# Optimization experiments

Measured on AMD Instinct MI355X. Metric: run time of the kernel, lower is better.

Reference implementation:

```python
import jax, jax.numpy as jnp
import numpy as np

EMBED = 1024
HEADS = 16
HEAD_DIM = EMBED // HEADS


def setup_inputs() -> dict:
    key = jax.random.key(0)
    k_x, k_qkv, k_ow, k_ob = jax.random.split(key, 4)
    B, N, D = 4, 2048, EMBED
    x = jax.random.normal(k_x, (B, N, D), dtype=jnp.float32)
    # nn.Linear stores weight as [out, in]; apply as x @ W.T
    s_in = 1.0 / np.sqrt(D)
    W_qkv = jax.random.uniform(k_qkv, (3 * D, D), dtype=jnp.float32, minval=-s_in, maxval=s_in)
    W_out = jax.random.uniform(k_ow, (D, D), dtype=jnp.float32, minval=-s_in, maxval=s_in)
    b_out = jax.random.uniform(k_ob, (D,), dtype=jnp.float32, minval=-s_in, maxval=s_in)
    return {"x": x, "W_qkv": W_qkv, "W_out": W_out, "b_out": b_out}


def reference(x, W_qkv, W_out, b_out):
    B, N, D = x.shape
    H, HD = HEADS, HEAD_DIM
    qkv = jnp.einsum("bnd,ed->bne", x, W_qkv)          # [B, N, 3D]
    qkv = qkv.reshape(B, N, 3, H, HD).transpose(2, 0, 3, 1, 4)  # [3, B, H, N, HD]
    q, k, v = qkv[0], qkv[1], qkv[2]
    scale = HD ** -0.5
    scores = jnp.einsum("bhnd,bhmd->bhnm", q, k) * scale  # [B, H, N, N]
    attn = jax.nn.softmax(scores, axis=-1)
    out = jnp.einsum("bhnm,bhmd->bhnd", attn, v)          # [B, H, N, HD]
    out = out.transpose(0, 2, 1, 3).reshape(B, N, D)
    return jnp.einsum("bnd,ed->bne", out, W_out) + b_out
```

## Files before the change

### kernel.cpp

```cpp
#include <hip/hip_runtime.h>
#include <hip/hip_bf16.h>
#include <stdint.h>

typedef float f32x4 __attribute__((ext_vector_type(4)));
typedef __bf16 v8bf __attribute__((ext_vector_type(8)));
typedef __bf16 v4bf __attribute__((ext_vector_type(4)));
typedef unsigned short u16x8 __attribute__((ext_vector_type(8)));

#define MFMA16 __builtin_amdgcn_mfma_f32_16x16x32_bf16

__device__ __forceinline__ void gload16(const void* g, void* l) {
  auto gp = reinterpret_cast<const __attribute__((address_space(1))) unsigned int*>(
      reinterpret_cast<uintptr_t>(g));
  auto lp = reinterpret_cast<__attribute__((address_space(3))) unsigned int*>(
      reinterpret_cast<uintptr_t>(l));
  __builtin_amdgcn_global_load_lds(gp, lp, 16, 0, 0);
}

__device__ __forceinline__ unsigned short f2bf(float f) {
  unsigned int u = __builtin_bit_cast(unsigned int, f);
  u += 0x7fffu + ((u >> 16) & 1u);
  return (unsigned short)(u >> 16);
}

__global__ __launch_bounds__(256) void cast_f32_bf16(const float* __restrict__ in,
                                                     unsigned short* __restrict__ out,
                                                     int n8) {
  int i = blockIdx.x * 256 + threadIdx.x;
  if (i >= n8) return;
  f32x4 a = *(const f32x4*)(in + (size_t)i * 8);
  f32x4 b = *(const f32x4*)(in + (size_t)i * 8 + 4);
  u16x8 v;
  v[0] = f2bf(a[0]); v[1] = f2bf(a[1]); v[2] = f2bf(a[2]); v[3] = f2bf(a[3]);
  v[4] = f2bf(b[0]); v[5] = f2bf(b[1]); v[6] = f2bf(b[2]); v[7] = f2bf(b[3]);
  *(u16x8*)(out + (size_t)i * 8) = v;
}

template <int EPI>
__global__ __launch_bounds__(256) void gemm_bt(const unsigned short* __restrict__ A,
                                               const unsigned short* __restrict__ Bw,
                                               unsigned short* __restrict__ Cb,
                                               float* __restrict__ Cf,
                                               const float* __restrict__ bias,
                                               int K, int nTilesN) {
  __shared__ __attribute__((aligned(16))) unsigned short As[128 * 64];
  __shared__ __attribute__((aligned(16))) unsigned short Bs[128 * 64];
  const int tid = threadIdx.x, lane = tid & 63, wv = tid >> 6;
  const int wr = wv >> 1, wc = wv & 1;
  const int l15 = lane & 15, lg = lane >> 4;
  const int m0 = (blockIdx.x / nTilesN) * 128;
  const int n0 = (blockIdx.x % nTilesN) * 128;

  f32x4 acc[4][4];
  const f32x4 z = {0.f, 0.f, 0.f, 0.f};
#pragma unroll
  for (int i = 0; i < 4; ++i)
#pragma unroll
    for (int j = 0; j < 4; ++j) acc[i][j] = z;

  const int jr = lane >> 3;
  const int c8 = (lane & 7) ^ jr;
  const unsigned short* Ag = A + (size_t)(m0 + wv * 32 + jr) * K + c8 * 8;
  const unsigned short* Bg = Bw + (size_t)(n0 + wv * 32 + jr) * K + c8 * 8;

  for (int kk = 0; kk < K; kk += 64) {
#pragma unroll
    for (int q4 = 0; q4 < 4; ++q4) {
      gload16(Ag + (size_t)q4 * 8 * K + kk, As + (wv * 4 + q4) * 512);
      gload16(Bg + (size_t)q4 * 8 * K + kk, Bs + (wv * 4 + q4) * 512);
    }
    __syncthreads();

    v8bf af[2][4], bfr[2][4];
#pragma unroll
    for (int mt = 0; mt < 4; ++mt) {
      const int r = wr * 64 + mt * 16 + l15;
      const int rx = r & 7;
      af[0][mt] = *(const v8bf*)(As + r * 64 + (lg ^ rx) * 8);
      af[1][mt] = *(const v8bf*)(As + r * 64 + ((4 + lg) ^ rx) * 8);
    }
#pragma unroll
    for (int nt = 0; nt < 4; ++nt) {
      const int r = wc * 64 + nt * 16 + l15;
      const int rx = r & 7;
      bfr[0][nt] = *(const v8bf*)(Bs + r * 64 + (lg ^ rx) * 8);
      bfr[1][nt] = *(const v8bf*)(Bs + r * 64 + ((4 + lg) ^ rx) * 8);
    }
#pragma unroll
    for (int mt = 0; mt < 4; ++mt)
#pragma unroll
      for (int nt = 0; nt < 4; ++nt) {
        acc[mt][nt] = MFMA16(af[0][mt], bfr[0][nt], acc[mt][nt], 0, 0, 0);
        acc[mt][nt] = MFMA16(af[1][mt], bfr[1][nt], acc[mt][nt], 0, 0, 0);
      }
    __syncthreads();
  }

#pragma unroll
  for (int mt = 0; mt < 4; ++mt)
#pragma unroll
    for (int nt = 0; nt < 4; ++nt)
#pragma unroll
      for (int r = 0; r < 4; ++r) {
        const int row = m0 + wr * 64 + mt * 16 + lg * 4 + r;
        const int col = n0 + wc * 64 + nt * 16 + l15;
        const float v = acc[mt][nt][r];
        if constexpr (EPI == 0) {
          const int mat = col >> 10, hc = col & 1023;
          const size_t dst =
              ((size_t)(mat * 64 + (row >> 11) * 16 + (hc >> 6)) * 2048 + (row & 2047)) * 64 +
              (hc & 63);
          Cb[dst] = f2bf(v);
        } else {
          Cf[(size_t)row * 1024 + col] = v + bias[col];
        }
      }
}

__global__ __launch_bounds__(256) void attn(const unsigned short* __restrict__ qkv,
                                            unsigned short* __restrict__ ao) {
  __shared__ __attribute__((aligned(16))) unsigned short Ks[64 * 64];
  __shared__ __attribute__((aligned(16))) unsigned short Vts[64][72];
  __shared__ __attribute__((aligned(16))) unsigned short Pl[4][16][64];
  const int bh = blockIdx.y;
  const int q0 = blockIdx.x * 64;
  const int tid = threadIdx.x, lane = tid & 63, wv = tid >> 6;
  const int l15 = lane & 15, lg = lane >> 4;
  const int a7 = l15 & 7;
  const size_t NH = (size_t)2048 * 64;
  const unsigned short* Qg = qkv + (size_t)bh * NH;
  const unsigned short* Kg = qkv + (size_t)(64 + bh) * NH;
  const unsigned short* Vg = qkv + (size_t)(128 + bh) * NH;

  const int qrow = q0 + wv * 16 + l15;
  const v8bf aq0 = *(const v8bf*)(Qg + (size_t)qrow * 64 + lg * 8);
  const v8bf aq1 = *(const v8bf*)(Qg + (size_t)qrow * 64 + 32 + lg * 8);

  const f32x4 z = {0.f, 0.f, 0.f, 0.f};
  float m_r = -3.0e38f, l_r = 0.f;
  f32x4 oacc[4];
#pragma unroll
  for (int dt = 0; dt < 4; ++dt) oacc[dt] = z;

  const float sc = 0.125f * 1.4426950408889634f;
  const float THR = 55.4f;
  const int jr = lane >> 3, c8 = (lane & 7) ^ jr;
  const int jp = tid & 31, dg = tid >> 5;

  for (int kv = 0; kv < 2048; kv += 64) {
    gload16(Kg + (size_t)(kv + wv * 16 + jr) * 64 + c8 * 8, Ks + (wv * 2) * 512);
    gload16(Kg + (size_t)(kv + wv * 16 + 8 + jr) * 64 + c8 * 8, Ks + (wv * 2 + 1) * 512);
    {
      u16x8 v0 = *(const u16x8*)(Vg + (size_t)(kv + 2 * jp) * 64 + dg * 8);
      u16x8 v1 = *(const u16x8*)(Vg + (size_t)(kv + 2 * jp + 1) * 64 + dg * 8);
#pragma unroll
      for (int e = 0; e < 8; ++e) {
        unsigned int pk = (unsigned int)v0[e] | ((unsigned int)v1[e] << 16);
        *(unsigned int*)&Vts[dg * 8 + e][2 * jp] = pk;
      }
    }
    __syncthreads();

    f32x4 s[4];
#pragma unroll
    for (int ct = 0; ct < 4; ++ct) {
      const int r = ct * 16 + l15, rx = r & 7;
      const v8bf kb0 = *(const v8bf*)(Ks + r * 64 + (lg ^ rx) * 8);
      const v8bf kb1 = *(const v8bf*)(Ks + r * 64 + ((4 + lg) ^ rx) * 8);
      s[ct] = MFMA16(kb0, aq0, z, 0, 0, 0);
      s[ct] = MFMA16(kb1, aq1, s[ct], 0, 0, 0);
    }

    float m01 = fmaxf(fmaxf(s[0][0], s[0][1]), fmaxf(s[0][2], s[0][3]));
    float m23 = fmaxf(fmaxf(s[1][0], s[1][1]), fmaxf(s[1][2], s[1][3]));
    float m45 = fmaxf(fmaxf(s[2][0], s[2][1]), fmaxf(s[2][2], s[2][3]));
    float m67 = fmaxf(fmaxf(s[3][0], s[3][1]), fmaxf(s[3][2], s[3][3]));
    float mx = fmaxf(fmaxf(m01, m23), fmaxf(m45, m67));
    mx = fmaxf(mx, __shfl_xor(mx, 16));
    mx = fmaxf(mx, __shfl_xor(mx, 32));

    if (__any(mx > m_r + THR)) {
      const float mn = fmaxf(m_r, mx);
      const float al = __builtin_amdgcn_exp2f((m_r - mn) * sc);
      m_r = mn;
      l_r *= al;
#pragma unroll
      for (int r = 0; r < 4; ++r) {
        const float a = __shfl(al, lg * 4 + r);
#pragma unroll
        for (int dt = 0; dt < 4; ++dt) oacc[dt][r] *= a;
      }
    }

    const float ms = m_r * sc;
    float p[4][4];
#pragma unroll
    for (int ct = 0; ct < 4; ++ct)
#pragma unroll
      for (int r = 0; r < 4; ++r)
        p[ct][r] = __builtin_amdgcn_exp2f(fmaf(s[ct][r], sc, -ms));
    float ps = ((p[0][0] + p[0][1]) + (p[0][2] + p[0][3])) +
               ((p[1][0] + p[1][1]) + (p[1][2] + p[1][3])) +
               ((p[2][0] + p[2][1]) + (p[2][2] + p[2][3])) +
               ((p[3][0] + p[3][1]) + (p[3][2] + p[3][3]));
    ps += __shfl_xor(ps, 16);
    ps += __shfl_xor(ps, 32);
    l_r += ps;

#pragma unroll
    for (int ct = 0; ct < 4; ++ct) {
      v4bf pk;
      pk[0] = (__bf16)p[ct][0]; pk[1] = (__bf16)p[ct][1];
      pk[2] = (__bf16)p[ct][2]; pk[3] = (__bf16)p[ct][3];
      const int cst = ct * 2 + (lg >> 1);
      *(v4bf*)(&Pl[wv][l15][((cst ^ a7) << 3) + ((lg & 1) << 2)]) = pk;
    }

    const v8bf pa0 = *(const v8bf*)(&Pl[wv][l15][(lg ^ a7) * 8]);
    const v8bf pa1 = *(const v8bf*)(&Pl[wv][l15][((4 + lg) ^ a7) * 8]);
#pragma unroll
    for (int dt = 0; dt < 4; ++dt) {
      const v8bf vb0 = *(const v8bf*)(&Vts[dt * 16 + l15][lg * 8]);
      const v8bf vb1 = *(const v8bf*)(&Vts[dt * 16 + l15][32 + lg * 8]);
      oacc[dt] = MFMA16(pa0, vb0, oacc[dt], 0, 0, 0);
      oacc[dt] = MFMA16(pa1, vb1, oacc[dt], 0, 0, 0);
    }
    __syncthreads();
  }

  const int b = bh >> 4, h = bh & 15;
  const float linv = 1.0f / l_r;
  float invr[4];
#pragma unroll
  for (int r = 0; r < 4; ++r) invr[r] = __shfl(linv, lg * 4 + r);
#pragma unroll
  for (int dt = 0; dt < 4; ++dt)
#pragma unroll
    for (int r = 0; r < 4; ++r) {
      const int row = q0 + wv * 16 + lg * 4 + r;
      const int col = h * 64 + dt * 16 + l15;
      ao[((size_t)b * 2048 + row) * 1024 + col] = f2bf(oacc[dt][r] * invr[r]);
    }
}

extern "C" void kernel_launch(void* const* d_in, const int* in_sizes, int n_in,
                              void* d_out, int out_size, void* d_ws, size_t ws_size,
                              hipStream_t stream) {
  (void)in_sizes; (void)n_in; (void)out_size; (void)ws_size;
  const float* x = (const float*)d_in[0];
  const float* Wqkv = (const float*)d_in[1];
  const float* Wout = (const float*)d_in[2];
  const float* bout = (const float*)d_in[3];
  float* out = (float*)d_out;

  char* ws = (char*)d_ws;
  unsigned short* Xb  = (unsigned short*)(ws);
  unsigned short* Wqb = (unsigned short*)(ws + (size_t)16 * 1048576);
  unsigned short* Wob = (unsigned short*)(ws + (size_t)22 * 1048576);
  unsigned short* QKV = (unsigned short*)(ws + (size_t)24 * 1048576);
  unsigned short* AO  = (unsigned short*)(ws + (size_t)72 * 1048576);

  cast_f32_bf16<<<4096, 256, 0, stream>>>(x, Xb, 1048576);
  cast_f32_bf16<<<1536, 256, 0, stream>>>(Wqkv, Wqb, 393216);
  cast_f32_bf16<<<512, 256, 0, stream>>>(Wout, Wob, 131072);
  gemm_bt<0><<<64 * 24, 256, 0, stream>>>(Xb, Wqb, QKV, nullptr, nullptr, 1024, 24);
  attn<<<dim3(32, 64), 256, 0, stream>>>(QKV, AO);
  gemm_bt<1><<<64 * 8, 256, 0, stream>>>(AO, Wob, nullptr, out, bout, 1024, 8);
}
```

Baseline: 333.4 us.

## Process two query tiles per wave in attention and swizzle GEMM block order

```diff
diff --git a/kernel.cpp b/kernel.cpp
--- a/kernel.cpp
+++ b/kernel.cpp
@@ -48,8 +48,11 @@
   const int tid = threadIdx.x, lane = tid & 63, wv = tid >> 6;
   const int wr = wv >> 1, wc = wv & 1;
   const int l15 = lane & 15, lg = lane >> 4;
-  const int m0 = (blockIdx.x / nTilesN) * 128;
-  const int n0 = (blockIdx.x % nTilesN) * 128;
+  const int nwg = gridDim.x;
+  int bid = blockIdx.x;
+  bid = (bid & 7) * (nwg >> 3) + (bid >> 3);
+  const int m0 = (bid / nTilesN) * 128;
+  const int n0 = (bid % nTilesN) * 128;
 
   f32x4 acc[4][4];
   const f32x4 z = {0.f, 0.f, 0.f, 0.f};
@@ -123,7 +126,7 @@
   __shared__ __attribute__((aligned(16))) unsigned short Vts[64][72];
   __shared__ __attribute__((aligned(16))) unsigned short Pl[4][16][64];
   const int bh = blockIdx.y;
-  const int q0 = blockIdx.x * 64;
+  const int q0 = blockIdx.x * 128;
   const int tid = threadIdx.x, lane = tid & 63, wv = tid >> 6;
   const int l15 = lane & 15, lg = lane >> 4;
   const int a7 = l15 & 7;
@@ -132,15 +135,20 @@
   const unsigned short* Kg = qkv + (size_t)(64 + bh) * NH;
   const unsigned short* Vg = qkv + (size_t)(128 + bh) * NH;
 
-  const int qrow = q0 + wv * 16 + l15;
-  const v8bf aq0 = *(const v8bf*)(Qg + (size_t)qrow * 64 + lg * 8);
-  const v8bf aq1 = *(const v8bf*)(Qg + (size_t)qrow * 64 + 32 + lg * 8);
+  const int qrow = q0 + wv * 32 + l15;
+  v8bf aq[2][2];
+  aq[0][0] = *(const v8bf*)(Qg + (size_t)qrow * 64 + lg * 8);
+  aq[0][1] = *(const v8bf*)(Qg + (size_t)qrow * 64 + 32 + lg * 8);
+  aq[1][0] = *(const v8bf*)(Qg + (size_t)(qrow + 16) * 64 + lg * 8);
+  aq[1][1] = *(const v8bf*)(Qg + (size_t)(qrow + 16) * 64 + 32 + lg * 8);
 
   const f32x4 z = {0.f, 0.f, 0.f, 0.f};
-  float m_r = -3.0e38f, l_r = 0.f;
-  f32x4 oacc[4];
-#pragma unroll
-  for (int dt = 0; dt < 4; ++dt) oacc[dt] = z;
+  float m_r[2] = {-3.0e38f, -3.0e38f}, l_r[2] = {0.f, 0.f};
+  f32x4 oacc[2][4];
+#pragma unroll
+  for (int g = 0; g < 2; ++g)
+#pragma unroll
+    for (int dt = 0; dt < 4; ++dt) oacc[g][dt] = z;
 
   const float sc = 0.125f * 1.4426950408889634f;
   const float THR = 55.4f;
@@ -161,86 +169,94 @@
     }
     __syncthreads();
 
-    f32x4 s[4];
+    f32x4 s[2][4];
 #pragma unroll
     for (int ct = 0; ct < 4; ++ct) {
       const int r = ct * 16 + l15, rx = r & 7;
       const v8bf kb0 = *(const v8bf*)(Ks + r * 64 + (lg ^ rx) * 8);
       const v8bf kb1 = *(const v8bf*)(Ks + r * 64 + ((4 + lg) ^ rx) * 8);
-      s[ct] = MFMA16(kb0, aq0, z, 0, 0, 0);
-      s[ct] = MFMA16(kb1, aq1, s[ct], 0, 0, 0);
-    }
-
-    float m01 = fmaxf(fmaxf(s[0][0], s[0][1]), fmaxf(s[0][2], s[0][3]));
-    float m23 = fmaxf(fmaxf(s[1][0], s[1][1]), fmaxf(s[1][2], s[1][3]));
-    float m45 = fmaxf(fmaxf(s[2][0], s[2][1]), fmaxf(s[2][2], s[2][3]));
-    float m67 = fmaxf(fmaxf(s[3][0], s[3][1]), fmaxf(s[3][2], s[3][3]));
-    float mx = fmaxf(fmaxf(m01, m23), fmaxf(m45, m67));
-    mx = fmaxf(mx, __shfl_xor(mx, 16));
-    mx = fmaxf(mx, __shfl_xor(mx, 32));
-
-    if (__any(mx > m_r + THR)) {
-      const float mn = fmaxf(m_r, mx);
-      const float al = __builtin_amdgcn_exp2f((m_r - mn) * sc);
-      m_r = mn;
-      l_r *= al;
+      s[0][ct] = MFMA16(kb0, aq[0][0], z, 0, 0, 0);
+      s[0][ct] = MFMA16(kb1, aq[0][1], s[0][ct], 0, 0, 0);
+      s[1][ct] = MFMA16(kb0, aq[1][0], z, 0, 0, 0);
+      s[1][ct] = MFMA16(kb1, aq[1][1], s[1][ct], 0, 0, 0);
+    }
+
+#pragma unroll
+    for (int g = 0; g < 2; ++g) {
+      float m01 = fmaxf(fmaxf(s[g][0][0], s[g][0][1]), fmaxf(s[g][0][2], s[g][0][3]));
+      float m23 = fmaxf(fmaxf(s[g][1][0], s[g][1][1]), fmaxf(s[g][1][2], s[g][1][3]));
+      float m45 = fmaxf(fmaxf(s[g][2][0], s[g][2][1]), fmaxf(s[g][2][2], s[g][2][3]));
+      float m67 = fmaxf(fmaxf(s[g][3][0], s[g][3][1]), fmaxf(s[g][3][2], s[g][3][3]));
+      float mx = fmaxf(fmaxf(m01, m23), fmaxf(m45, m67));
+      mx = fmaxf(mx, __shfl_xor(mx, 16));
+      mx = fmaxf(mx, __shfl_xor(mx, 32));
+
+      if (__any(mx > m_r[g] + THR)) {
+        const float mn = fmaxf(m_r[g], mx);
+        const float al = __builtin_amdgcn_exp2f((m_r[g] - mn) * sc);
+        m_r[g] = mn;
+        l_r[g] *= al;
+#pragma unroll
+        for (int r = 0; r < 4; ++r) {
+          const float a = __shfl(al, lg * 4 + r);
+#pragma unroll
+          for (int dt = 0; dt < 4; ++dt) oacc[g][dt][r] *= a;
+        }
+      }
+
+      const float ms = m_r[g] * sc;
+      float p[4][4];
+#pragma unroll
+      for (int ct = 0; ct < 4; ++ct)
+#pragma unroll
+        for (int r = 0; r < 4; ++r)
+          p[ct][r] = __builtin_amdgcn_exp2f(fmaf(s[g][ct][r], sc, -ms));
+      float ps = ((p[0][0] + p[0][1]) + (p[0][2] + p[0][3])) +
+                 ((p[1][0] + p[1][1]) + (p[1][2] + p[1][3])) +
+                 ((p[2][0] + p[2][1]) + (p[2][2] + p[2][3])) +
+                 ((p[3][0] + p[3][1]) + (p[3][2] + p[3][3]));
+      ps += __shfl_xor(ps, 16);
+      ps += __shfl_xor(ps, 32);
+      l_r[g] += ps;
+
+#pragma unroll
+      for (int ct = 0; ct < 4; ++ct) {
+        v4bf pk;
+        pk[0] = (__bf16)p[ct][0]; pk[1] = (__bf16)p[ct][1];
+        pk[2] = (__bf16)p[ct][2]; pk[3] = (__bf16)p[ct][3];
+        const int cst = ct * 2 + (lg >> 1);
+        *(v4bf*)(&Pl[wv][l15][((cst ^ a7) << 3) + ((lg & 1) << 2)]) = pk;
+      }
+
+      const v8bf pa0 = *(const v8bf*)(&Pl[wv][l15][(lg ^ a7) * 8]);
+      const v8bf pa1 = *(const v8bf*)(&Pl[wv][l15][((4 + lg) ^ a7) * 8]);
+#pragma unroll
+      for (int dt = 0; dt < 4; ++dt) {
+        const v8bf vb0 = *(const v8bf*)(&Vts[dt * 16 + l15][lg * 8]);
+        const v8bf vb1 = *(const v8bf*)(&Vts[dt * 16 + l15][32 + lg * 8]);
+        oacc[g][dt] = MFMA16(pa0, vb0, oacc[g][dt], 0, 0, 0);
+        oacc[g][dt] = MFMA16(pa1, vb1, oacc[g][dt], 0, 0, 0);
+      }
+    }
+    __syncthreads();
+  }
+
+  const int b = bh >> 4, h = bh & 15;
+#pragma unroll
+  for (int g = 0; g < 2; ++g) {
+    const float linv = 1.0f / l_r[g];
+    float invr[4];
+#pragma unroll
+    for (int r = 0; r < 4; ++r) invr[r] = __shfl(linv, lg * 4 + r);
+#pragma unroll
+    for (int dt = 0; dt < 4; ++dt)
 #pragma unroll
       for (int r = 0; r < 4; ++r) {
-        const float a = __shfl(al, lg * 4 + r);
-#pragma unroll
-        for (int dt = 0; dt < 4; ++dt) oacc[dt][r] *= a;
-      }
-    }
-
-    const float ms = m_r * sc;
-    float p[4][4];
-#pragma unroll
-    for (int ct = 0; ct < 4; ++ct)
-#pragma unroll
-      for (int r = 0; r < 4; ++r)
-        p[ct][r] = __builtin_amdgcn_exp2f(fmaf(s[ct][r], sc, -ms));
-    float ps = ((p[0][0] + p[0][1]) + (p[0][2] + p[0][3])) +
-               ((p[1][0] + p[1][1]) + (p[1][2] + p[1][3])) +
-               ((p[2][0] + p[2][1]) + (p[2][2] + p[2][3])) +
-               ((p[3][0] + p[3][1]) + (p[3][2] + p[3][3]));
-    ps += __shfl_xor(ps, 16);
-    ps += __shfl_xor(ps, 32);
-    l_r += ps;
-
-#pragma unroll
-    for (int ct = 0; ct < 4; ++ct) {
-      v4bf pk;
-      pk[0] = (__bf16)p[ct][0]; pk[1] = (__bf16)p[ct][1];
-      pk[2] = (__bf16)p[ct][2]; pk[3] = (__bf16)p[ct][3];
-      const int cst = ct * 2 + (lg >> 1);
-      *(v4bf*)(&Pl[wv][l15][((cst ^ a7) << 3) + ((lg & 1) << 2)]) = pk;
-    }
-
-    const v8bf pa0 = *(const v8bf*)(&Pl[wv][l15][(lg ^ a7) * 8]);
-    const v8bf pa1 = *(const v8bf*)(&Pl[wv][l15][((4 + lg) ^ a7) * 8]);
-#pragma unroll
-    for (int dt = 0; dt < 4; ++dt) {
-      const v8bf vb0 = *(const v8bf*)(&Vts[dt * 16 + l15][lg * 8]);
-      const v8bf vb1 = *(const v8bf*)(&Vts[dt * 16 + l15][32 + lg * 8]);
-      oacc[dt] = MFMA16(pa0, vb0, oacc[dt], 0, 0, 0);
-      oacc[dt] = MFMA16(pa1, vb1, oacc[dt], 0, 0, 0);
-    }
-    __syncthreads();
+        const int row = q0 + wv * 32 + g * 16 + lg * 4 + r;
+        const int col = h * 64 + dt * 16 + l15;
+        ao[((size_t)b * 2048 + row) * 1024 + col] = f2bf(oacc[g][dt][r] * invr[r]);
+      }
   }
-
-  const int b = bh >> 4, h = bh & 15;
-  const float linv = 1.0f / l_r;
-  float invr[4];
-#pragma unroll
-  for (int r = 0; r < 4; ++r) invr[r] = __shfl(linv, lg * 4 + r);
-#pragma unroll
-  for (int dt = 0; dt < 4; ++dt)
-#pragma unroll
-    for (int r = 0; r < 4; ++r) {
-      const int row = q0 + wv * 16 + lg * 4 + r;
-      const int col = h * 64 + dt * 16 + l15;
-      ao[((size_t)b * 2048 + row) * 1024 + col] = f2bf(oacc[dt][r] * invr[r]);
-    }
 }
 
 extern "C" void kernel_launch(void* const* d_in, const int* in_sizes, int n_in,
@@ -264,6 +280,6 @@
   cast_f32_bf16<<<1536, 256, 0, stream>>>(Wqkv, Wqb, 393216);
   cast_f32_bf16<<<512, 256, 0, stream>>>(Wout, Wob, 131072);
   gemm_bt<0><<<64 * 24, 256, 0, stream>>>(Xb, Wqb, QKV, nullptr, nullptr, 1024, 24);
-  attn<<<dim3(32, 64), 256, 0, stream>>>(QKV, AO);
+  attn<<<dim3(16, 64), 256, 0, stream>>>(QKV, AO);
   gemm_bt<1><<<64 * 8, 256, 0, stream>>>(AO, Wob, nullptr, out, bout, 1024, 8);
 }
```

Result: faster. 325.7 us (-2.3%).
